# Kernel optimization log

Hardware: AMD Instinct MI355X
Metric: run time of the kernel (lower is better)

Reference implementation:

```python
import jax, jax.numpy as jnp
import numpy as np


def setup_inputs() -> dict:
    key = jax.random.key(0)
    x = jax.random.normal(key, (4096, 4096), dtype=jnp.float32)
    # upsample factor encoded as the length of factor_token (dtype matches x)
    factor_token = jnp.ones((2,), dtype=jnp.float32)
    return {"x": x, "factor_token": factor_token}


def reference(x, factor_token):
    # FFT-based 2D upsampling: FFT -> centered zero-pad in frequency domain -> iFFT.
    f = factor_token.shape[0]  # static upsample factor (token length)
    H, W = x.shape
    Hn, Wn = H * f, W * f
    # forward 2D FFT, shift DC to center for symmetric zero-padding
    X = jnp.fft.fftshift(jnp.fft.fft2(x))  # complex [H, W]
    ph0 = (Hn - H) // 2
    pw0 = (Wn - W) // 2
    Xp = jnp.zeros((Hn, Wn), dtype=X.dtype).at[ph0:ph0 + H, pw0:pw0 + W].set(X)
    # inverse FFT; scale by f*f to preserve signal amplitude (FFT normalization)
    y = jnp.fft.ifft2(jnp.fft.ifftshift(Xp)) * (f * f)
    return jnp.real(y).astype(x.dtype)
```

## Files before the change

kernel.cpp:

```cpp
#include <hip/hip_runtime.h>
#include <math.h>

#define N   4096
#define NO  8192
#define TBL_ELEMS (128 * 128 * 32)

#ifndef M_PI
#define M_PI 3.14159265358979323846
#endif

typedef __attribute__((ext_vector_type(8))) short short8;
typedef __attribute__((ext_vector_type(4))) float f32x4;


__device__ __forceinline__ unsigned bf16h(float f) {
    unsigned u = __float_as_uint(f);
    return (u + 0x7FFFu + ((u >> 16) & 1u)) >> 16;
}

__global__ void init_weights_kernel(float* w) {
    int m = blockIdx.x * blockDim.x + threadIdx.x;
    if (m < N) {
        double ang = M_PI * (2.0 * (double)m + 1.0) / (2.0 * (double)N);
        double v = (cos(ang) / sin(ang)) / (double)N;
        w[m] = (m & 1) ? (float)(-v) : (float)v;
    }
    if (blockIdx.x == 0 && threadIdx.x == 0) w[N] = 0.0f;
}

__global__ void build_table_kernel(const float* __restrict__ wf,
                                   ushort* __restrict__ th, ushort* __restrict__ tl) {
    int idx = blockIdx.x * 256 + threadIdx.x;
    int k = idx & 31;
    int r = (idx >> 5) & 127;
    int g = idx >> 12;
    int m = (r - k - 32 * g) & (N - 1);
    float f = wf[m];
    unsigned h = bf16h(f);
    float hf = __uint_as_float(h << 16);
    unsigned l = bf16h(f - hf);
    th[idx] = (ushort)h;
    tl[idx] = (ushort)l;
}

__global__ void reduce_sign_kernel(const float* __restrict__ x, float* S) {
    const size_t NN = (size_t)N * N;
    float acc = 0.0f;
    for (size_t idx = (size_t)blockIdx.x * blockDim.x + threadIdx.x; idx < NN;
         idx += (size_t)gridDim.x * blockDim.x) {
        int st = (int)((idx >> 12) + (idx & (N - 1)));
        float v = x[idx];
        acc += (st & 1) ? -v : v;
    }
    #pragma unroll
    for (int off = 32; off > 0; off >>= 1) acc += __shfl_down(acc, off, 64);
    __shared__ float wsum[4];
    int lane = threadIdx.x & 63;
    int wv   = threadIdx.x >> 6;
    if (lane == 0) wsum[wv] = acc;
    __syncthreads();
    if (threadIdx.x == 0) atomicAdd(S, wsum[0] + wsum[1] + wsum[2] + wsum[3]);
}

__device__ __forceinline__ void split8(const float4& a0, const float4& a1,
                                       short8& hi, short8& lo) {
    float av[8] = {a0.x, a0.y, a0.z, a0.w, a1.x, a1.y, a1.z, a1.w};
    #pragma unroll
    for (int j = 0; j < 8; ++j) {
        unsigned h = bf16h(av[j]);
        float hf = __uint_as_float(h << 16);
        hi[j] = (short)h;
        lo[j] = (short)bf16h(av[j] - hf);
    }
}

__global__ __launch_bounds__(256) void hpass_mfma(const float* __restrict__ x,
                                                  const ushort* __restrict__ th,
                                                  const ushort* __restrict__ tl,
                                                  float* __restrict__ out) {
    const int j0 = blockIdx.x * 128;
    const int s0 = blockIdx.y * 128;
    const int tid = threadIdx.x;
    const int w   = tid >> 6;
    const int l   = tid & 63;
    const int lr  = l & 15;
    const int kb  = (l >> 4) * 8;
    const int wm  = (w >> 1) * 64;
    const int wn  = (w & 1) * 64;

    f32x4 acc[4][4];
    #pragma unroll
    for (int a = 0; a < 4; ++a)
        #pragma unroll
        for (int b = 0; b < 4; ++b)
            acc[a][b] = (f32x4){0.f, 0.f, 0.f, 0.f};

    for (int t0 = 0; t0 < N; t0 += 32) {
        const int g = ((t0 - j0) & (N - 1)) >> 5;
        short8 bh[4], bl[4];
        #pragma unroll
        for (int nf = 0; nf < 4; ++nf) {
            int r = wn + nf * 16 + lr;
            size_t flat = ((size_t)(g * 128 + r) << 5) + kb;
            bh[nf] = *reinterpret_cast<const short8*>(th + flat);
            bl[nf] = *reinterpret_cast<const short8*>(tl + flat);
        }
        #pragma unroll
        for (int mf = 0; mf < 4; ++mf) {
            const float* ap = x + (size_t)(s0 + wm + mf * 16 + lr) * N + (t0 + kb);
            float4 a0 = *reinterpret_cast<const float4*>(ap);
            float4 a1 = *reinterpret_cast<const float4*>(ap + 4);
            short8 ah, al;
            split8(a0, a1, ah, al);
            #pragma unroll
            for (int nf = 0; nf < 4; ++nf) {
                acc[mf][nf] = __builtin_amdgcn_mfma_f32_16x16x32_bf16(ah, bh[nf], acc[mf][nf], 0, 0, 0);
                acc[mf][nf] = __builtin_amdgcn_mfma_f32_16x16x32_bf16(ah, bl[nf], acc[mf][nf], 0, 0, 0);
                acc[mf][nf] = __builtin_amdgcn_mfma_f32_16x16x32_bf16(al, bh[nf], acc[mf][nf], 0, 0, 0);
            }
        }
    }

    const int crow = (l >> 4) * 4;
    #pragma unroll
    for (int mf = 0; mf < 4; ++mf) {
        #pragma unroll
        for (int i = 0; i < 4; ++i) {
            int s = s0 + wm + mf * 16 + crow + i;
            #pragma unroll
            for (int nf = 0; nf < 4; ++nf) {
                int j = j0 + wn + nf * 16 + lr;
                float xv = x[(size_t)s * N + j];
                float2 v2 = make_float2(xv, acc[mf][nf][i]);
                *reinterpret_cast<float2*>(out + (size_t)(2 * s) * NO + (size_t)(2 * j)) = v2;
            }
        }
    }
}

__global__ __launch_bounds__(256) void vpass_mfma(const ushort* __restrict__ th,
                                                  const ushort* __restrict__ tl,
                                                  const float* __restrict__ S,
                                                  float* out) {
    const int i0 = blockIdx.x * 128;
    const int b0 = blockIdx.y * 128;
    const int tid = threadIdx.x;
    const int w   = tid >> 6;
    const int l   = tid & 63;
    const int lr  = l & 15;
    const int kb  = (l >> 4) * 8;
    const int wm  = (w >> 1) * 64;
    const int wn  = (w & 1) * 64;

    f32x4 acc[4][4];
    #pragma unroll
    for (int a = 0; a < 4; ++a)
        #pragma unroll
        for (int b = 0; b < 4; ++b)
            acc[a][b] = (f32x4){0.f, 0.f, 0.f, 0.f};

    for (int s0 = 0; s0 < N; s0 += 32) {
        short8 bh[4], bl[4];
        #pragma unroll
        for (int nf = 0; nf < 4; ++nf) {
            int colb = b0 + wn + nf * 16 + lr;
            const float* ep = out + (size_t)(2 * (s0 + kb)) * NO + colb;
            float ev[8];
            #pragma unroll
            for (int j = 0; j < 8; ++j)
                ev[j] = ep[(size_t)(2 * j) * NO];
            #pragma unroll
            for (int j = 0; j < 8; ++j) {
                unsigned h = bf16h(ev[j]);
                float hf = __uint_as_float(h << 16);
                bh[nf][j] = (short)h;
                bl[nf][j] = (short)bf16h(ev[j] - hf);
            }
        }
        const int g = ((s0 - i0) & (N - 1)) >> 5;
        #pragma unroll
        for (int mf = 0; mf < 4; ++mf) {
            int r = wm + mf * 16 + lr;
            size_t flat = ((size_t)(g * 128 + r) << 5) + kb;
            short8 ah = *reinterpret_cast<const short8*>(th + flat);
            short8 al = *reinterpret_cast<const short8*>(tl + flat);
            #pragma unroll
            for (int nf = 0; nf < 4; ++nf) {
                acc[mf][nf] = __builtin_amdgcn_mfma_f32_16x16x32_bf16(ah, bh[nf], acc[mf][nf], 0, 0, 0);
                acc[mf][nf] = __builtin_amdgcn_mfma_f32_16x16x32_bf16(ah, bl[nf], acc[mf][nf], 0, 0, 0);
                acc[mf][nf] = __builtin_amdgcn_mfma_f32_16x16x32_bf16(al, bh[nf], acc[mf][nf], 0, 0, 0);
            }
        }
    }

    const float Sval = S[0] * (1.0f / ((float)N * (float)N));
    const int crow = (l >> 4) * 4;
    #pragma unroll
    for (int mf = 0; mf < 4; ++mf) {
        #pragma unroll
        for (int i = 0; i < 4; ++i) {
            int irow = i0 + wm + mf * 16 + crow + i;
            #pragma unroll
            for (int nf = 0; nf < 4; ++nf) {
                int b = b0 + wn + nf * 16 + lr;
                float v = acc[mf][nf][i];
                if (b & 1) {
                    int jdx = (b - 1) >> 1;
                    v -= (((irow + jdx) & 1) ? -Sval : Sval);
                }
                out[(size_t)(2 * irow + 1) * NO + (size_t)b] = v;
            }
        }
    }
}

extern "C" void kernel_launch(void* const* d_in, const int* in_sizes, int n_in,
                              void* d_out, int out_size, void* d_ws, size_t ws_size,
                              hipStream_t stream) {
    const float* x = (const float*)d_in[0];
    float* out = (float*)d_out;
    float* wf = (float*)d_ws;
    ushort* th = (ushort*)(wf + 4352);
    ushort* tl = th + TBL_ELEMS;

    init_weights_kernel<<<(N + 255) / 256, 256, 0, stream>>>(wf);
    build_table_kernel<<<TBL_ELEMS / 256, 256, 0, stream>>>(wf, th, tl);
    reduce_sign_kernel<<<1024, 256, 0, stream>>>(x, wf + N);

    dim3 hgrid(N / 128, N / 128);
    hpass_mfma<<<hgrid, 256, 0, stream>>>(x, th, tl, out);

    dim3 vgrid(N / 128, NO / 128);
    vpass_mfma<<<vgrid, 256, 0, stream>>>(th, tl, wf + N, out);
}
```

Before: 2.172 ms.

## Precompute bf16 hi/lo splits and transposed intermediates in workspace for both passes

Adds a conversion kernel that splits x into bf16 hi/lo planes once, writes a transposed split copy for the vertical pass, and folds the sign reduction into it. The horizontal pass then loads pre-split operands and writes a transposed hi/lo copy of its result, so the vertical pass reads contiguous short8 vectors instead of eight strided fp32 loads plus conversions. MFMA issue is also regrouped into three independent sweeps. This costs extra workspace and extra global writes, and falls back to the old on-the-fly path when the workspace is too small.

```diff
diff --git a/kernel.cpp b/kernel.cpp
--- a/kernel.cpp
+++ b/kernel.cpp
@@ -11,6 +11,7 @@
 
 typedef __attribute__((ext_vector_type(8))) short short8;
 typedef __attribute__((ext_vector_type(4))) float f32x4;
+typedef __attribute__((ext_vector_type(4))) unsigned short u16x4;
 
 
 __device__ __forceinline__ unsigned bf16h(float f) {
@@ -62,22 +63,57 @@
     if (threadIdx.x == 0) atomicAdd(S, wsum[0] + wsum[1] + wsum[2] + wsum[3]);
 }
 
-__device__ __forceinline__ void split8(const float4& a0, const float4& a1,
-                                       short8& hi, short8& lo) {
-    float av[8] = {a0.x, a0.y, a0.z, a0.w, a1.x, a1.y, a1.z, a1.w};
-    #pragma unroll
-    for (int j = 0; j < 8; ++j) {
-        unsigned h = bf16h(av[j]);
+__global__ __launch_bounds__(256) void convert_x_kernel(const float* __restrict__ x,
+        ushort* __restrict__ xh, ushort* __restrict__ xl,
+        ushort* __restrict__ ETh, ushort* __restrict__ ETl, float* __restrict__ S) {
+    __shared__ uint tile[32][33];
+    __shared__ float wsum[4];
+    const int bj = blockIdx.x * 32;
+    const int bs = blockIdx.y * 32;
+    const int tid = threadIdx.x;
+    const int row = tid >> 3;
+    const int c4  = (tid & 7) << 2;
+
+    float4 v = *reinterpret_cast<const float4*>(x + (size_t)(bs + row) * N + bj + c4);
+    float av[4] = {v.x, v.y, v.z, v.w};
+    u16x4 h4, l4;
+    float sacc = 0.0f;
+    #pragma unroll
+    for (int i = 0; i < 4; ++i) {
+        unsigned h = bf16h(av[i]);
         float hf = __uint_as_float(h << 16);
-        hi[j] = (short)h;
-        lo[j] = (short)bf16h(av[j] - hf);
-    }
-}
-
-__global__ __launch_bounds__(256) void hpass_mfma(const float* __restrict__ x,
-                                                  const ushort* __restrict__ th,
-                                                  const ushort* __restrict__ tl,
-                                                  float* __restrict__ out) {
+        unsigned lo = bf16h(av[i] - hf);
+        h4[i] = (unsigned short)h;
+        l4[i] = (unsigned short)lo;
+        tile[row][c4 + i] = (h << 16) | lo;
+        sacc += (((bs + row) + (bj + c4 + i)) & 1) ? -av[i] : av[i];
+    }
+    size_t ro = (size_t)(bs + row) * N + bj + c4;
+    *reinterpret_cast<u16x4*>(xh + ro) = h4;
+    *reinterpret_cast<u16x4*>(xl + ro) = l4;
+
+    #pragma unroll
+    for (int off = 32; off > 0; off >>= 1) sacc += __shfl_down(sacc, off, 64);
+    if ((tid & 63) == 0) wsum[tid >> 6] = sacc;
+    __syncthreads();
+    if (tid == 0) atomicAdd(S, wsum[0] + wsum[1] + wsum[2] + wsum[3]);
+
+    u16x4 th4, tl4;
+    #pragma unroll
+    for (int i = 0; i < 4; ++i) {
+        uint p = tile[c4 + i][row];
+        th4[i] = (unsigned short)(p >> 16);
+        tl4[i] = (unsigned short)(p & 0xFFFFu);
+    }
+    size_t eo = (size_t)(2 * (bj + row)) * N + bs + c4;
+    *reinterpret_cast<u16x4*>(ETh + eo) = th4;
+    *reinterpret_cast<u16x4*>(ETl + eo) = tl4;
+}
+
+__global__ __launch_bounds__(256) void hpass_pre(const float* __restrict__ x,
+        const ushort* __restrict__ xh, const ushort* __restrict__ xl,
+        const ushort* __restrict__ th, const ushort* __restrict__ tl,
+        float* __restrict__ out, ushort* __restrict__ ETh, ushort* __restrict__ ETl) {
     const int j0 = blockIdx.x * 128;
     const int s0 = blockIdx.y * 128;
     const int tid = threadIdx.x;
@@ -97,51 +133,64 @@
 
     for (int t0 = 0; t0 < N; t0 += 32) {
         const int g = ((t0 - j0) & (N - 1)) >> 5;
-        short8 bh[4], bl[4];
+        short8 bh[4], bl[4], ah[4], al[4];
         #pragma unroll
         for (int nf = 0; nf < 4; ++nf) {
-            int r = wn + nf * 16 + lr;
-            size_t flat = ((size_t)(g * 128 + r) << 5) + kb;
+            size_t flat = ((size_t)(g * 128 + wn + nf * 16 + lr) << 5) + kb;
             bh[nf] = *reinterpret_cast<const short8*>(th + flat);
             bl[nf] = *reinterpret_cast<const short8*>(tl + flat);
         }
         #pragma unroll
         for (int mf = 0; mf < 4; ++mf) {
-            const float* ap = x + (size_t)(s0 + wm + mf * 16 + lr) * N + (t0 + kb);
-            float4 a0 = *reinterpret_cast<const float4*>(ap);
-            float4 a1 = *reinterpret_cast<const float4*>(ap + 4);
-            short8 ah, al;
-            split8(a0, a1, ah, al);
-            #pragma unroll
-            for (int nf = 0; nf < 4; ++nf) {
-                acc[mf][nf] = __builtin_amdgcn_mfma_f32_16x16x32_bf16(ah, bh[nf], acc[mf][nf], 0, 0, 0);
-                acc[mf][nf] = __builtin_amdgcn_mfma_f32_16x16x32_bf16(ah, bl[nf], acc[mf][nf], 0, 0, 0);
-                acc[mf][nf] = __builtin_amdgcn_mfma_f32_16x16x32_bf16(al, bh[nf], acc[mf][nf], 0, 0, 0);
-            }
-        }
+            size_t ao = (size_t)(s0 + wm + mf * 16 + lr) * N + t0 + kb;
+            ah[mf] = *reinterpret_cast<const short8*>(xh + ao);
+            al[mf] = *reinterpret_cast<const short8*>(xl + ao);
+        }
+        #pragma unroll
+        for (int mf = 0; mf < 4; ++mf)
+            #pragma unroll
+            for (int nf = 0; nf < 4; ++nf)
+                acc[mf][nf] = __builtin_amdgcn_mfma_f32_16x16x32_bf16(ah[mf], bh[nf], acc[mf][nf], 0, 0, 0);
+        #pragma unroll
+        for (int mf = 0; mf < 4; ++mf)
+            #pragma unroll
+            for (int nf = 0; nf < 4; ++nf)
+                acc[mf][nf] = __builtin_amdgcn_mfma_f32_16x16x32_bf16(ah[mf], bl[nf], acc[mf][nf], 0, 0, 0);
+        #pragma unroll
+        for (int mf = 0; mf < 4; ++mf)
+            #pragma unroll
+            for (int nf = 0; nf < 4; ++nf)
+                acc[mf][nf] = __builtin_amdgcn_mfma_f32_16x16x32_bf16(al[mf], bh[nf], acc[mf][nf], 0, 0, 0);
     }
 
     const int crow = (l >> 4) * 4;
     #pragma unroll
     for (int mf = 0; mf < 4; ++mf) {
-        #pragma unroll
-        for (int i = 0; i < 4; ++i) {
-            int s = s0 + wm + mf * 16 + crow + i;
-            #pragma unroll
-            for (int nf = 0; nf < 4; ++nf) {
-                int j = j0 + wn + nf * 16 + lr;
-                float xv = x[(size_t)s * N + j];
-                float2 v2 = make_float2(xv, acc[mf][nf][i]);
-                *reinterpret_cast<float2*>(out + (size_t)(2 * s) * NO + (size_t)(2 * j)) = v2;
-            }
-        }
-    }
-}
-
-__global__ __launch_bounds__(256) void vpass_mfma(const ushort* __restrict__ th,
-                                                  const ushort* __restrict__ tl,
-                                                  const float* __restrict__ S,
-                                                  float* out) {
+        const int sbase = s0 + wm + mf * 16 + crow;
+        #pragma unroll
+        for (int nf = 0; nf < 4; ++nf) {
+            const int j = j0 + wn + nf * 16 + lr;
+            u16x4 h4, l4;
+            #pragma unroll
+            for (int i = 0; i < 4; ++i) {
+                float zv = acc[mf][nf][i];
+                float xv = x[(size_t)(sbase + i) * N + j];
+                *reinterpret_cast<float2*>(out + (size_t)(2 * (sbase + i)) * NO + (size_t)(2 * j)) =
+                    make_float2(xv, zv);
+                unsigned h = bf16h(zv);
+                h4[i] = (unsigned short)h;
+                l4[i] = (unsigned short)bf16h(zv - __uint_as_float(h << 16));
+            }
+            size_t eo = (size_t)(2 * j + 1) * N + sbase;
+            *reinterpret_cast<u16x4*>(ETh + eo) = h4;
+            *reinterpret_cast<u16x4*>(ETl + eo) = l4;
+        }
+    }
+}
+
+__global__ __launch_bounds__(256) void vpass_pre(const ushort* __restrict__ th,
+        const ushort* __restrict__ tl, const ushort* __restrict__ ETh,
+        const ushort* __restrict__ ETl, const float* __restrict__ S, float* __restrict__ out) {
     const int i0 = blockIdx.x * 128;
     const int b0 = blockIdx.y * 128;
     const int tid = threadIdx.x;
@@ -160,37 +209,35 @@
             acc[a][b] = (f32x4){0.f, 0.f, 0.f, 0.f};
 
     for (int s0 = 0; s0 < N; s0 += 32) {
-        short8 bh[4], bl[4];
+        short8 bh[4], bl[4], ah[4], al[4];
         #pragma unroll
         for (int nf = 0; nf < 4; ++nf) {
-            int colb = b0 + wn + nf * 16 + lr;
-            const float* ep = out + (size_t)(2 * (s0 + kb)) * NO + colb;
-            float ev[8];
-            #pragma unroll
-            for (int j = 0; j < 8; ++j)
-                ev[j] = ep[(size_t)(2 * j) * NO];
-            #pragma unroll
-            for (int j = 0; j < 8; ++j) {
-                unsigned h = bf16h(ev[j]);
-                float hf = __uint_as_float(h << 16);
-                bh[nf][j] = (short)h;
-                bl[nf][j] = (short)bf16h(ev[j] - hf);
-            }
+            size_t eo = (size_t)(b0 + wn + nf * 16 + lr) * N + s0 + kb;
+            bh[nf] = *reinterpret_cast<const short8*>(ETh + eo);
+            bl[nf] = *reinterpret_cast<const short8*>(ETl + eo);
         }
         const int g = ((s0 - i0) & (N - 1)) >> 5;
         #pragma unroll
         for (int mf = 0; mf < 4; ++mf) {
-            int r = wm + mf * 16 + lr;
-            size_t flat = ((size_t)(g * 128 + r) << 5) + kb;
-            short8 ah = *reinterpret_cast<const short8*>(th + flat);
-            short8 al = *reinterpret_cast<const short8*>(tl + flat);
-            #pragma unroll
-            for (int nf = 0; nf < 4; ++nf) {
-                acc[mf][nf] = __builtin_amdgcn_mfma_f32_16x16x32_bf16(ah, bh[nf], acc[mf][nf], 0, 0, 0);
-                acc[mf][nf] = __builtin_amdgcn_mfma_f32_16x16x32_bf16(ah, bl[nf], acc[mf][nf], 0, 0, 0);
-                acc[mf][nf] = __builtin_amdgcn_mfma_f32_16x16x32_bf16(al, bh[nf], acc[mf][nf], 0, 0, 0);
-            }
-        }
+            size_t flat = ((size_t)(g * 128 + wm + mf * 16 + lr) << 5) + kb;
+            ah[mf] = *reinterpret_cast<const short8*>(th + flat);
+            al[mf] = *reinterpret_cast<const short8*>(tl + flat);
+        }
+        #pragma unroll
+        for (int mf = 0; mf < 4; ++mf)
+            #pragma unroll
+            for (int nf = 0; nf < 4; ++nf)
+                acc[mf][nf] = __builtin_amdgcn_mfma_f32_16x16x32_bf16(ah[mf], bh[nf], acc[mf][nf], 0, 0, 0);
+        #pragma unroll
+        for (int mf = 0; mf < 4; ++mf)
+            #pragma unroll
+            for (int nf = 0; nf < 4; ++nf)
+                acc[mf][nf] = __builtin_amdgcn_mfma_f32_16x16x32_bf16(ah[mf], bl[nf], acc[mf][nf], 0, 0, 0);
+        #pragma unroll
+        for (int mf = 0; mf < 4; ++mf)
+            #pragma unroll
+            for (int nf = 0; nf < 4; ++nf)
+                acc[mf][nf] = __builtin_amdgcn_mfma_f32_16x16x32_bf16(al[mf], bh[nf], acc[mf][nf], 0, 0, 0);
     }
 
     const float Sval = S[0] * (1.0f / ((float)N * (float)N));
@@ -214,22 +261,163 @@
     }
 }
 
+__device__ __forceinline__ void split8(const float4& a0, const float4& a1,
+                                       short8& hi, short8& lo) {
+    float av[8] = {a0.x, a0.y, a0.z, a0.w, a1.x, a1.y, a1.z, a1.w};
+    #pragma unroll
+    for (int j = 0; j < 8; ++j) {
+        unsigned h = bf16h(av[j]);
+        float hf = __uint_as_float(h << 16);
+        hi[j] = (short)h;
+        lo[j] = (short)bf16h(av[j] - hf);
+    }
+}
+
+__global__ __launch_bounds__(256) void hpass_fly(const float* __restrict__ x,
+        const ushort* __restrict__ th, const ushort* __restrict__ tl,
+        float* __restrict__ out) {
+    const int j0 = blockIdx.x * 128;
+    const int s0 = blockIdx.y * 128;
+    const int tid = threadIdx.x;
+    const int w = tid >> 6, l = tid & 63;
+    const int lr = l & 15, kb = (l >> 4) * 8;
+    const int wm = (w >> 1) * 64, wn = (w & 1) * 64;
+    f32x4 acc[4][4];
+    #pragma unroll
+    for (int a = 0; a < 4; ++a)
+        #pragma unroll
+        for (int b = 0; b < 4; ++b) acc[a][b] = (f32x4){0.f, 0.f, 0.f, 0.f};
+    for (int t0 = 0; t0 < N; t0 += 32) {
+        const int g = ((t0 - j0) & (N - 1)) >> 5;
+        short8 bh[4], bl[4];
+        #pragma unroll
+        for (int nf = 0; nf < 4; ++nf) {
+            size_t flat = ((size_t)(g * 128 + wn + nf * 16 + lr) << 5) + kb;
+            bh[nf] = *reinterpret_cast<const short8*>(th + flat);
+            bl[nf] = *reinterpret_cast<const short8*>(tl + flat);
+        }
+        #pragma unroll
+        for (int mf = 0; mf < 4; ++mf) {
+            const float* ap = x + (size_t)(s0 + wm + mf * 16 + lr) * N + (t0 + kb);
+            float4 a0 = *reinterpret_cast<const float4*>(ap);
+            float4 a1 = *reinterpret_cast<const float4*>(ap + 4);
+            short8 ah, al;
+            split8(a0, a1, ah, al);
+            #pragma unroll
+            for (int nf = 0; nf < 4; ++nf) {
+                acc[mf][nf] = __builtin_amdgcn_mfma_f32_16x16x32_bf16(ah, bh[nf], acc[mf][nf], 0, 0, 0);
+                acc[mf][nf] = __builtin_amdgcn_mfma_f32_16x16x32_bf16(ah, bl[nf], acc[mf][nf], 0, 0, 0);
+                acc[mf][nf] = __builtin_amdgcn_mfma_f32_16x16x32_bf16(al, bh[nf], acc[mf][nf], 0, 0, 0);
+            }
+        }
+    }
+    const int crow = (l >> 4) * 4;
+    #pragma unroll
+    for (int mf = 0; mf < 4; ++mf)
+        #pragma unroll
+        for (int i = 0; i < 4; ++i) {
+            int s = s0 + wm + mf * 16 + crow + i;
+            #pragma unroll
+            for (int nf = 0; nf < 4; ++nf) {
+                int j = j0 + wn + nf * 16 + lr;
+                float xv = x[(size_t)s * N + j];
+                *reinterpret_cast<float2*>(out + (size_t)(2 * s) * NO + (size_t)(2 * j)) =
+                    make_float2(xv, acc[mf][nf][i]);
+            }
+        }
+}
+
+__global__ __launch_bounds__(256) void vpass_fly(const ushort* __restrict__ th,
+        const ushort* __restrict__ tl, const float* __restrict__ S, float* out) {
+    const int i0 = blockIdx.x * 128;
+    const int b0 = blockIdx.y * 128;
+    const int tid = threadIdx.x;
+    const int w = tid >> 6, l = tid & 63;
+    const int lr = l & 15, kb = (l >> 4) * 8;
+    const int wm = (w >> 1) * 64, wn = (w & 1) * 64;
+    f32x4 acc[4][4];
+    #pragma unroll
+    for (int a = 0; a < 4; ++a)
+        #pragma unroll
+        for (int b = 0; b < 4; ++b) acc[a][b] = (f32x4){0.f, 0.f, 0.f, 0.f};
+    for (int s0 = 0; s0 < N; s0 += 32) {
+        short8 bh[4], bl[4];
+        #pragma unroll
+        for (int nf = 0; nf < 4; ++nf) {
+            int colb = b0 + wn + nf * 16 + lr;
+            const float* ep = out + (size_t)(2 * (s0 + kb)) * NO + colb;
+            float ev[8];
+            #pragma unroll
+            for (int j = 0; j < 8; ++j) ev[j] = ep[(size_t)(2 * j) * NO];
+            #pragma unroll
+            for (int j = 0; j < 8; ++j) {
+                unsigned h = bf16h(ev[j]);
+                float hf = __uint_as_float(h << 16);
+                bh[nf][j] = (short)h;
+                bl[nf][j] = (short)bf16h(ev[j] - hf);
+            }
+        }
+        const int g = ((s0 - i0) & (N - 1)) >> 5;
+        #pragma unroll
+        for (int mf = 0; mf < 4; ++mf) {
+            size_t flat = ((size_t)(g * 128 + wm + mf * 16 + lr) << 5) + kb;
+            short8 ah = *reinterpret_cast<const short8*>(th + flat);
+            short8 al = *reinterpret_cast<const short8*>(tl + flat);
+            #pragma unroll
+            for (int nf = 0; nf < 4; ++nf) {
+                acc[mf][nf] = __builtin_amdgcn_mfma_f32_16x16x32_bf16(ah, bh[nf], acc[mf][nf], 0, 0, 0);
+                acc[mf][nf] = __builtin_amdgcn_mfma_f32_16x16x32_bf16(ah, bl[nf], acc[mf][nf], 0, 0, 0);
+                acc[mf][nf] = __builtin_amdgcn_mfma_f32_16x16x32_bf16(al, bh[nf], acc[mf][nf], 0, 0, 0);
+            }
+        }
+    }
+    const float Sval = S[0] * (1.0f / ((float)N * (float)N));
+    const int crow = (l >> 4) * 4;
+    #pragma unroll
+    for (int mf = 0; mf < 4; ++mf)
+        #pragma unroll
+        for (int i = 0; i < 4; ++i) {
+            int irow = i0 + wm + mf * 16 + crow + i;
+            #pragma unroll
+            for (int nf = 0; nf < 4; ++nf) {
+                int b = b0 + wn + nf * 16 + lr;
+                float v = acc[mf][nf][i];
+                if (b & 1) {
+                    int jdx = (b - 1) >> 1;
+                    v -= (((irow + jdx) & 1) ? -Sval : Sval);
+                }
+                out[(size_t)(2 * irow + 1) * NO + (size_t)b] = v;
+            }
+        }
+}
+
 extern "C" void kernel_launch(void* const* d_in, const int* in_sizes, int n_in,
                               void* d_out, int out_size, void* d_ws, size_t ws_size,
                               hipStream_t stream) {
     const float* x = (const float*)d_in[0];
     float* out = (float*)d_out;
-    float* wf = (float*)d_ws;
-    ushort* th = (ushort*)(wf + 4352);
+    char* base = (char*)d_ws;
+    float* wf = (float*)base;
+    ushort* th = (ushort*)(base + 65536);
     ushort* tl = th + TBL_ELEMS;
 
+    const size_t need = 65536 + (size_t)4 * TBL_ELEMS
+                      + (size_t)4 * N * N
+                      + (size_t)4 * NO * N;
     init_weights_kernel<<<(N + 255) / 256, 256, 0, stream>>>(wf);
     build_table_kernel<<<TBL_ELEMS / 256, 256, 0, stream>>>(wf, th, tl);
-    reduce_sign_kernel<<<1024, 256, 0, stream>>>(x, wf + N);
-
-    dim3 hgrid(N / 128, N / 128);
-    hpass_mfma<<<hgrid, 256, 0, stream>>>(x, th, tl, out);
-
-    dim3 vgrid(N / 128, NO / 128);
-    vpass_mfma<<<vgrid, 256, 0, stream>>>(th, tl, wf + N, out);
-}
+
+    if (ws_size >= need) {
+        ushort* xh  = (ushort*)(base + 65536 + (size_t)4 * TBL_ELEMS);
+        ushort* xl  = xh + (size_t)N * N;
+        ushort* ETh = xl + (size_t)N * N;
+        ushort* ETl = ETh + (size_t)NO * N;
+        convert_x_kernel<<<dim3(N / 32, N / 32), 256, 0, stream>>>(x, xh, xl, ETh, ETl, wf + N);
+        hpass_pre<<<dim3(N / 128, N / 128), 256, 0, stream>>>(x, xh, xl, th, tl, out, ETh, ETl);
+        vpass_pre<<<dim3(N / 128, NO / 128), 256, 0, stream>>>(th, tl, ETh, ETl, wf + N, out);
+    } else {
+        reduce_sign_kernel<<<1024, 256, 0, stream>>>(x, wf + N);
+        hpass_fly<<<dim3(N / 128, N / 128), 256, 0, stream>>>(x, th, tl, out);
+        vpass_fly<<<dim3(N / 128, NO / 128), 256, 0, stream>>>(th, tl, wf + N, out);
+    }
+}
```

After: 2.877 ms. 1.32x slower.
